# Kernel optimization log

Hardware: AMD Instinct MI355X
Metric: run time of the kernel (lower is better)

Reference implementation:

```python
import jax, jax.numpy as jnp
import numpy as np

B, T, C = 2, 2048, 1024
H = 16
DK = C // H


def setup_inputs() -> dict:
    key = jax.random.key(0)
    ks = jax.random.split(key, 5)
    x = jax.random.normal(ks[0], (B, T, C), dtype=jnp.float32)
    # causal mask, broadcastable to [B, H, T, T]; mask==0 -> -inf
    mask = jnp.tril(jnp.ones((T, T), dtype=jnp.int32))[None, None]
    s = 1.0 / np.sqrt(C)
    qkv_w = jax.random.normal(ks[1], (3 * C, C), dtype=jnp.float32) * s  # torch Linear layout [out,in]
    qkv_b = jnp.zeros((3 * C,), dtype=jnp.float32)
    out_w = jax.random.normal(ks[2], (C, C), dtype=jnp.float32) * s
    out_b = jnp.zeros((C,), dtype=jnp.float32)
    return {"x": x, "mask": mask, "qkv_w": qkv_w, "qkv_b": qkv_b,
            "out_w": out_w, "out_b": out_b}


def reference(x, mask, qkv_w, qkv_b, out_w, out_b):
    b, t, c = x.shape
    qkv = x @ qkv_w.T + qkv_b                       # [B,T,3C]
    qkv = qkv.reshape(b, t, 3, H, DK)
    q, k, v = qkv[:, :, 0], qkv[:, :, 1], qkv[:, :, 2]   # [B,T,H,DK]
    scores = jnp.einsum('bqhd,bkhd->bhqk', q, k) / np.sqrt(DK)
    scores = jnp.where(mask == 0, -jnp.inf, scores)
    attn_weights = jax.nn.softmax(scores, axis=-1)       # [B,H,T,T]
    attn_out = jnp.einsum('bhqk,bkhd->bqhd', attn_weights, v).reshape(b, t, c)
    out = attn_out @ out_w.T + out_b
    return out, attn_weights
```

## Files before the change

### kernel.cpp

```cpp
#include <hip/hip_runtime.h>
#include <hip/hip_bf16.h>

typedef short short8  __attribute__((ext_vector_type(8)));
typedef short short4v __attribute__((ext_vector_type(4)));
typedef __bf16 bf16x8 __attribute__((ext_vector_type(8)));
typedef float f32x4   __attribute__((ext_vector_type(4)));

__device__ __forceinline__ void mfma16(f32x4& d, short8 a, short8 b) {
    d = __builtin_amdgcn_mfma_f32_16x16x32_bf16(
            __builtin_bit_cast(bf16x8, a), __builtin_bit_cast(bf16x8, b), d, 0, 0, 0);
}

__device__ __forceinline__ unsigned short f2bf(float f) {
    __bf16 b = (__bf16)f;
    return __builtin_bit_cast(unsigned short, b);
}
__device__ __forceinline__ float bf2f(unsigned short us) {
    union { unsigned u; float f; } a; a.u = ((unsigned)us) << 16;
    return a.f;
}

__global__ void cvt_all(const float* __restrict__ x, const float* __restrict__ w1,
                        const float* __restrict__ w2,
                        unsigned short* __restrict__ ox, unsigned short* __restrict__ o1,
                        unsigned short* __restrict__ o2) {
    int i = blockIdx.x * 256 + threadIdx.x;
    const float* src; unsigned short* dst; int j;
    if (i < 1048576)      { src = x;  dst = ox; j = i; }
    else if (i < 1835008) { src = w1; dst = o1; j = i - 1048576; }
    else                  { src = w2; dst = o2; j = i - 1835008; }
    float4 v = ((const float4*)src)[j];
    ushort4 o;
    o.x = f2bf(v.x); o.y = f2bf(v.y); o.z = f2bf(v.z); o.w = f2bf(v.w);
    ((ushort4*)dst)[j] = o;
}

template<int OUTBF, int VTF, int BM, int BN, int MAP>
__global__ __launch_bounds__(256)
void gemm_bt(const unsigned short* __restrict__ A, const unsigned short* __restrict__ Bw,
             const float* __restrict__ bias, void* __restrict__ Cout,
             unsigned short* __restrict__ vt, unsigned short* __restrict__ khb,
             int M, int N, int K)
{
    constexpr int MM = BM / 32;
    constexpr int NN = BN / 32;
    __shared__ unsigned short As[BM * 64];
    __shared__ unsigned short Bs[BN * 64];

    const int tid  = threadIdx.x;
    const int lane = tid & 63;
    const int wid  = tid >> 6;

    int row0, col0;
    if constexpr (MAP == 1) {
        const int xcd = blockIdx.x & 7, lid = blockIdx.x >> 3;
        const int super = lid / 24, sub = lid % 24;
        row0 = ((super << 3) + (sub & 7)) << 7;
        col0 = (xcd * 3 + (sub >> 3)) << 7;
    } else {
        const int xcd = blockIdx.x & 7, lid = blockIdx.x >> 3;
        row0 = (lid >> 1) << 7;
        col0 = ((xcd << 1) + (lid & 1)) << 6;
    }
    const int wr = (wid >> 1) * (BM >> 1);
    const int wc = (wid & 1) * (BN >> 1);
    const int rl = lane & 15;
    const int g  = lane >> 4;

    f32x4 acc[MM][NN] = {};

    for (int k0 = 0; k0 < K; k0 += 64) {
        __syncthreads();
#pragma unroll
        for (int rd = 0; rd < (BM >> 5); ++rd) {
            int s  = rd * 256 + tid;
            int r  = s >> 3, cs = s & 7;
            int cg = cs ^ (r & 7);
            __builtin_amdgcn_global_load_lds(
                (__attribute__((address_space(1))) void*)(A + (size_t)(row0 + r) * K + k0 + cg * 8),
                (__attribute__((address_space(3))) void*)(As + s * 8), 16, 0, 0);
        }
#pragma unroll
        for (int rd = 0; rd < (BN >> 5); ++rd) {
            int s  = rd * 256 + tid;
            int r  = s >> 3, cs = s & 7;
            int cg = cs ^ (r & 7);
            __builtin_amdgcn_global_load_lds(
                (__attribute__((address_space(1))) void*)(Bw + (size_t)(col0 + r) * K + k0 + cg * 8),
                (__attribute__((address_space(3))) void*)(Bs + s * 8), 16, 0, 0);
        }
        __syncthreads();

#pragma unroll
        for (int h = 0; h < 2; ++h) {
            short8 af[MM], bf[NN];
#pragma unroll
            for (int m = 0; m < MM; ++m) {
                int rr = wr + m * 16 + rl;
                int ch = ((h << 2) + g) ^ (rr & 7);
                af[m] = *(const short8*)(As + rr * 64 + ch * 8);
            }
#pragma unroll
            for (int n = 0; n < NN; ++n) {
                int rr = wc + n * 16 + rl;
                int ch = ((h << 2) + g) ^ (rr & 7);
                bf[n] = *(const short8*)(Bs + rr * 64 + ch * 8);
            }
#pragma unroll
            for (int m = 0; m < MM; ++m)
#pragma unroll
                for (int n = 0; n < NN; ++n)
                    mfma16(acc[m][n], af[m], bf[n]);
        }
    }

    const int b  = row0 >> 11;
    const int tg = (row0 & 2047) + wr + (g << 2);
#pragma unroll
    for (int n = 0; n < NN; ++n) {
        int col = col0 + wc + n * 16 + rl;
        float bv = bias[col];
        if (VTF && col >= 2048) {
            int hd = col - 2048;
            unsigned short* vr = vt + ((size_t)((b << 4) + (hd >> 6)) * 64 + (hd & 63)) * 2048;
#pragma unroll
            for (int m = 0; m < MM; ++m) {
                short4v p;
#pragma unroll
                for (int r = 0; r < 4; ++r) p[r] = (short)f2bf(acc[m][n][r] + bv);
                *(short4v*)(vr + tg + m * 16) = p;
            }
        } else if (VTF && col >= 1024) {
            int hd = col - 1024;
            unsigned short* kr = khb + ((size_t)((b << 4) + (hd >> 6)) << 17) + (hd & 63);
#pragma unroll
            for (int m = 0; m < MM; ++m)
#pragma unroll
                for (int r = 0; r < 4; ++r)
                    kr[(size_t)(tg + m * 16 + r) << 6] = f2bf(acc[m][n][r] + bv);
        } else if (VTF) {
#pragma unroll
            for (int m = 0; m < MM; ++m)
#pragma unroll
                for (int r = 0; r < 4; ++r)
                    ((unsigned short*)Cout)[(size_t)(row0 + wr + m * 16 + (g << 2) + r) * 1024 + col]
                        = f2bf(acc[m][n][r] + bv);
        } else {
#pragma unroll
            for (int m = 0; m < MM; ++m) {
#pragma unroll
                for (int r = 0; r < 4; ++r) {
                    int row = row0 + wr + m * 16 + (g << 2) + r;
                    float v = acc[m][n][r] + bv;
                    if (OUTBF) ((unsigned short*)Cout)[(size_t)row * N + col] = f2bf(v);
                    else       ((float*)Cout)[(size_t)row * N + col] = v;
                }
            }
        }
    }
}

__device__ __forceinline__ int S_addr(int row, int col) {
    return (row << 11) + ((((col >> 3) ^ (row & 7))) << 3) + (col & 7);
}

__global__ __launch_bounds__(256, 2)
void attn_kernel(const unsigned short* __restrict__ qbuf,
                 const unsigned short* __restrict__ khb,
                 const unsigned short* __restrict__ vt,
                 float* __restrict__ wout,
                 unsigned short* __restrict__ aout)
{
    __shared__ unsigned short Ss[16 * 2048];
    __shared__ float part[4][16];

    const int bid = (int)(((blockIdx.x & 7) << 9) + (blockIdx.x >> 3));
    const int qt = bid & 127;
    const int bh = bid >> 7;
    const int b = bh >> 4, h = bh & 15;
    const int q0 = qt << 4;
    const int tid = threadIdx.x;
    const int wid = tid >> 6;
    const int lane = tid & 63;
    const int rl = lane & 15;
    const int g  = lane >> 4;

    int nt = (qt + 4) & ~3;
    if (nt > 128) nt = 128;
    const int ntiles = nt;
    const int KPAD = ntiles << 4;

    const unsigned short* Qb = qbuf + (size_t)((b << 11) + q0) * 1024 + (h << 6);
    short8 qf0 = *(const short8*)(Qb + rl * 1024 + g * 8);
    short8 qf1 = *(const short8*)(Qb + rl * 1024 + 32 + g * 8);

    const unsigned short* Kh = khb + ((size_t)bh << 17);

    float psum[4] = {0.f, 0.f, 0.f, 0.f};

    {
        short8 ka0, ka1, kb0, kb1;
        {
            const unsigned short* kp = Kh + (size_t)((wid * 16 + rl) << 6);
            ka0 = *(const short8*)(kp + g * 8);
            ka1 = *(const short8*)(kp + 32 + g * 8);
        }
        if (wid + 4 < ntiles) {
            const unsigned short* kp = Kh + (size_t)((((wid + 4) * 16) + rl) << 6);
            kb0 = *(const short8*)(kp + g * 8);
            kb1 = *(const short8*)(kp + 32 + g * 8);
        } else { kb0 = ka0; kb1 = ka1; }
        for (int kt = wid; kt < ntiles; kt += 4) {
            short8 kc0 = ka0, kc1 = ka1;
            ka0 = kb0; ka1 = kb1;
            if (kt + 8 < ntiles) {
                const unsigned short* kp2 = Kh + (size_t)((((kt + 8) * 16) + rl) << 6);
                kb0 = *(const short8*)(kp2 + g * 8);
                kb1 = *(const short8*)(kp2 + 32 + g * 8);
            }
            f32x4 acc = {};
            __builtin_amdgcn_s_setprio(1);
            mfma16(acc, qf0, kc0);
            mfma16(acc, qf1, kc1);
            __builtin_amdgcn_s_setprio(0);
            int col = kt * 16 + rl;
#pragma unroll
            for (int r = 0; r < 4; ++r) {
                int qrow = g * 4 + r;
                float e = (col <= q0 + qrow) ? __expf(acc[r] * 0.125f) : 0.0f;
                Ss[S_addr(qrow, col)] = f2bf(e);
                psum[r] += e;
            }
        }
    }
#pragma unroll
    for (int m = 8; m; m >>= 1)
#pragma unroll
        for (int r = 0; r < 4; ++r) psum[r] += __shfl_xor(psum[r], m);
    if (rl == 0) {
#pragma unroll
        for (int r = 0; r < 4; ++r) part[wid][g * 4 + r] = psum[r];
    }
    __syncthreads();

    f32x4 p0 = {}, p1 = {};
    const unsigned short* vrow = vt + ((size_t)(bh << 6) + wid * 16 + rl) * 2048;
    const int np = KPAD >> 6;
    const int wrow = wid + (g << 2);
    const float invw = 1.0f / (part[0][wrow] + part[1][wrow] + part[2][wrow] + part[3][wrow]);
    float* worow = wout + ((size_t)bh * 2048 + q0 + wrow) * 2048;
    short8 bv0 = *(const short8*)(vrow + (g << 3));
    short8 bv1 = *(const short8*)(vrow + 32 + (g << 3));
    for (int ic = 0; ic < 32; ++ic) {
        int colb = (ic << 6) + (rl << 2);
        f32x4 o;
        if (ic < np) {
            short8 c0 = bv0, c1 = bv1;
            if (ic + 1 < np) {
                bv0 = *(const short8*)(vrow + ((ic + 1) << 6) + (g << 3));
                bv1 = *(const short8*)(vrow + ((ic + 1) << 6) + 32 + (g << 3));
            }
            int k0c = (ic << 3) + g;
            short8 a0 = *(const short8*)(Ss + (rl << 11) + ((k0c ^ (rl & 7)) << 3));
            short8 a1 = *(const short8*)(Ss + (rl << 11) + (((k0c + 4) ^ (rl & 7)) << 3));
            __builtin_amdgcn_s_setprio(1);
            mfma16(p0, a0, c0);
            mfma16(p1, a1, c1);
            __builtin_amdgcn_s_setprio(0);
            short4v sv = *(const short4v*)(Ss + S_addr(wrow, colb));
            o[0] = bf2f((unsigned short)sv[0]) * invw;
            o[1] = bf2f((unsigned short)sv[1]) * invw;
            o[2] = bf2f((unsigned short)sv[2]) * invw;
            o[3] = bf2f((unsigned short)sv[3]) * invw;
        } else {
            o[0] = 0.f; o[1] = 0.f; o[2] = 0.f; o[3] = 0.f;
        }
        __builtin_nontemporal_store(o, (f32x4*)(worow + colb));
    }

    f32x4 pacc = p0 + p1;
#pragma unroll
    for (int r = 0; r < 4; ++r) {
        int qrow = g * 4 + r;
        float inv = 1.0f / (part[0][qrow] + part[1][qrow] + part[2][qrow] + part[3][qrow]);
        float v = pacc[r] * inv;
        aout[(size_t)((b << 11) + q0 + qrow) * 1024 + (h << 6) + wid * 16 + rl] = f2bf(v);
    }
}

extern "C" void kernel_launch(void* const* d_in, const int* in_sizes, int n_in,
                              void* d_out, int out_size, void* d_ws, size_t ws_size,
                              hipStream_t stream)
{
    const float* x     = (const float*)d_in[0];
    const float* qkv_w = (const float*)d_in[2];
    const float* qkv_b = (const float*)d_in[3];
    const float* out_w = (const float*)d_in[4];
    const float* out_b = (const float*)d_in[5];

    char* ws = (char*)d_ws;
    unsigned short* xbf   = (unsigned short*)(ws);
    unsigned short* wqkv  = (unsigned short*)(ws + 8388608);
    unsigned short* woutw = (unsigned short*)(ws + 14680064);
    unsigned short* qbuf  = (unsigned short*)(ws + 16777216);
    unsigned short* vt    = (unsigned short*)(ws + 25165824);
    unsigned short* aout  = (unsigned short*)(ws + 33554432);
    unsigned short* khb   = (unsigned short*)(ws + 41943040);

    float* out  = (float*)d_out;
    float* wout = (float*)d_out + 4194304;

    cvt_all<<<8192, 256, 0, stream>>>(x, qkv_w, out_w, xbf, wqkv, woutw);

    gemm_bt<1, 1, 128, 128, 1><<<768, 256, 0, stream>>>(xbf, wqkv, qkv_b, qbuf, vt, khb, 4096, 3072, 1024);
    attn_kernel<<<4096, 256, 0, stream>>>(qbuf, khb, vt, wout, aout);
    gemm_bt<0, 0, 128, 64, 3><<<512, 256, 0, stream>>>(aout, woutw, out_b, out, nullptr, nullptr, 4096, 1024, 1024);
}
```

Baseline: 213.4 us.

## Double-buffer GEMM K-loop with async LDS staging and reverse attention tile order

Measured after the change: 230.9 us. 8.2% more time.

```diff
diff --git a/kernel.cpp b/kernel.cpp
--- a/kernel.cpp
+++ b/kernel.cpp
@@ -18,6 +18,25 @@
 __device__ __forceinline__ float bf2f(unsigned short us) {
     union { unsigned u; float f; } a; a.u = ((unsigned)us) << 16;
     return a.f;
+}
+
+template<int ROWS>
+__device__ __forceinline__ void stage32(const unsigned short* __restrict__ src,
+                                        unsigned short* lds, int row0, int K, int k0, int tid) {
+#pragma unroll
+    for (int rd = 0; rd < (ROWS >> 6); ++rd) {
+        int s = rd * 256 + tid;
+        int p = s >> 3, cs = s & 7;
+        int cg = cs ^ (p & 7);
+        __builtin_amdgcn_global_load_lds(
+            (__attribute__((address_space(1))) void*)(src + (size_t)(row0 + 2 * p + (cg >> 2)) * K + k0 + (cg & 3) * 8),
+            (__attribute__((address_space(3))) void*)(lds + s * 8), 16, 0, 0);
+    }
+}
+__device__ __forceinline__ short8 frag32(const unsigned short* buf, int rr, int g) {
+    int p = rr >> 1;
+    int ch = (((rr & 1) << 2) | g) ^ (p & 7);
+    return *(const short8*)(buf + p * 64 + ch * 8);
 }
 
 __global__ void cvt_all(const float* __restrict__ x, const float* __restrict__ w1,
@@ -44,8 +63,9 @@
 {
     constexpr int MM = BM / 32;
     constexpr int NN = BN / 32;
-    __shared__ unsigned short As[BM * 64];
-    __shared__ unsigned short Bs[BN * 64];
+    constexpr int LPT = (BM + BN) / 64;
+    __shared__ unsigned short As[2][BM * 32];
+    __shared__ unsigned short Bs[2][BN * 32];
 
     const int tid  = threadIdx.x;
     const int lane = tid & 63;
@@ -69,48 +89,38 @@
 
     f32x4 acc[MM][NN] = {};
 
-    for (int k0 = 0; k0 < K; k0 += 64) {
-        __syncthreads();
-#pragma unroll
-        for (int rd = 0; rd < (BM >> 5); ++rd) {
-            int s  = rd * 256 + tid;
-            int r  = s >> 3, cs = s & 7;
-            int cg = cs ^ (r & 7);
-            __builtin_amdgcn_global_load_lds(
-                (__attribute__((address_space(1))) void*)(A + (size_t)(row0 + r) * K + k0 + cg * 8),
-                (__attribute__((address_space(3))) void*)(As + s * 8), 16, 0, 0);
-        }
-#pragma unroll
-        for (int rd = 0; rd < (BN >> 5); ++rd) {
-            int s  = rd * 256 + tid;
-            int r  = s >> 3, cs = s & 7;
-            int cg = cs ^ (r & 7);
-            __builtin_amdgcn_global_load_lds(
-                (__attribute__((address_space(1))) void*)(Bw + (size_t)(col0 + r) * K + k0 + cg * 8),
-                (__attribute__((address_space(3))) void*)(Bs + s * 8), 16, 0, 0);
-        }
-        __syncthreads();
-
-#pragma unroll
-        for (int h = 0; h < 2; ++h) {
-            short8 af[MM], bf[NN];
-#pragma unroll
-            for (int m = 0; m < MM; ++m) {
-                int rr = wr + m * 16 + rl;
-                int ch = ((h << 2) + g) ^ (rr & 7);
-                af[m] = *(const short8*)(As + rr * 64 + ch * 8);
-            }
-#pragma unroll
-            for (int n = 0; n < NN; ++n) {
-                int rr = wc + n * 16 + rl;
-                int ch = ((h << 2) + g) ^ (rr & 7);
-                bf[n] = *(const short8*)(Bs + rr * 64 + ch * 8);
-            }
-#pragma unroll
-            for (int m = 0; m < MM; ++m)
-#pragma unroll
-                for (int n = 0; n < NN; ++n)
-                    mfma16(acc[m][n], af[m], bf[n]);
+    const int NT = K >> 5;
+    stage32<BM>(A,  As[0], row0, K, 0,  tid);
+    stage32<BN>(Bw, Bs[0], col0, K, 0,  tid);
+    stage32<BM>(A,  As[1], row0, K, 32, tid);
+    stage32<BN>(Bw, Bs[1], col0, K, 32, tid);
+
+    for (int t = 0; t < NT; ++t) {
+        const int cur = t & 1;
+        if (t + 1 < NT) {
+            asm volatile("s_waitcnt vmcnt(%0)" :: "i"(LPT) : "memory");
+        } else {
+            asm volatile("s_waitcnt vmcnt(0)" ::: "memory");
+        }
+        __builtin_amdgcn_s_barrier();
+
+        short8 af[MM], bf[NN];
+#pragma unroll
+        for (int m = 0; m < MM; ++m) af[m] = frag32(As[cur], wr + m * 16 + rl, g);
+#pragma unroll
+        for (int n = 0; n < NN; ++n) bf[n] = frag32(Bs[cur], wc + n * 16 + rl, g);
+        __builtin_amdgcn_s_setprio(1);
+#pragma unroll
+        for (int m = 0; m < MM; ++m)
+#pragma unroll
+            for (int n = 0; n < NN; ++n)
+                mfma16(acc[m][n], af[m], bf[n]);
+        __builtin_amdgcn_s_setprio(0);
+
+        __builtin_amdgcn_s_barrier();
+        if (t + 2 < NT) {
+            stage32<BM>(A,  As[cur], row0, K, (t + 2) << 5, tid);
+            stage32<BN>(Bw, Bs[cur], col0, K, (t + 2) << 5, tid);
         }
     }
 
@@ -175,7 +185,7 @@
     __shared__ float part[4][16];
 
     const int bid = (int)(((blockIdx.x & 7) << 9) + (blockIdx.x >> 3));
-    const int qt = bid & 127;
+    const int qt = 127 - (bid & 127);
     const int bh = bid >> 7;
     const int b = bh >> 4, h = bh & 15;
     const int q0 = qt << 4;
```

## Halve attention query tile to 8 rows and shrink output-projection GEMM tiles

Applied to the files above, without the earlier changes.

New measurement: 330.0 us. +54.6%, slower.

```diff
diff --git a/kernel.cpp b/kernel.cpp
--- a/kernel.cpp
+++ b/kernel.cpp
@@ -5,6 +5,7 @@
 typedef short short4v __attribute__((ext_vector_type(4)));
 typedef __bf16 bf16x8 __attribute__((ext_vector_type(8)));
 typedef float f32x4   __attribute__((ext_vector_type(4)));
+typedef float f32x2   __attribute__((ext_vector_type(2)));
 
 __device__ __forceinline__ void mfma16(f32x4& d, short8 a, short8 b) {
     d = __builtin_amdgcn_mfma_f32_16x16x32_bf16(
@@ -59,7 +60,7 @@
         col0 = (xcd * 3 + (sub >> 3)) << 7;
     } else {
         const int xcd = blockIdx.x & 7, lid = blockIdx.x >> 3;
-        row0 = (lid >> 1) << 7;
+        row0 = (lid >> 1) << 6;
         col0 = ((xcd << 1) + (lid & 1)) << 6;
     }
     const int wr = (wid >> 1) * (BM >> 1);
@@ -164,31 +165,32 @@
     return (row << 11) + ((((col >> 3) ^ (row & 7))) << 3) + (col & 7);
 }
 
-__global__ __launch_bounds__(256, 2)
+__global__ __launch_bounds__(256, 4)
 void attn_kernel(const unsigned short* __restrict__ qbuf,
                  const unsigned short* __restrict__ khb,
                  const unsigned short* __restrict__ vt,
                  float* __restrict__ wout,
                  unsigned short* __restrict__ aout)
 {
-    __shared__ unsigned short Ss[16 * 2048];
+    __shared__ unsigned short Ss[8 * 2048];
     __shared__ float part[4][16];
 
-    const int bid = (int)(((blockIdx.x & 7) << 9) + (blockIdx.x >> 3));
-    const int qt = bid & 127;
-    const int bh = bid >> 7;
+    const int bid = (int)(((blockIdx.x & 7) << 10) + (blockIdx.x >> 3));
+    const int qt8 = bid & 255;
+    const int bh = bid >> 8;
     const int b = bh >> 4, h = bh & 15;
-    const int q0 = qt << 4;
+    const int q0 = qt8 << 3;
     const int tid = threadIdx.x;
     const int wid = tid >> 6;
     const int lane = tid & 63;
     const int rl = lane & 15;
     const int g  = lane >> 4;
 
-    int nt = (qt + 4) & ~3;
+    int nt = ((qt8 >> 1) + 4) & ~3;
     if (nt > 128) nt = 128;
     const int ntiles = nt;
     const int KPAD = ntiles << 4;
+    const int np = KPAD >> 6;
 
     const unsigned short* Qb = qbuf + (size_t)((b << 11) + q0) * 1024 + (h << 6);
     short8 qf0 = *(const short8*)(Qb + rl * 1024 + g * 8);
@@ -224,12 +226,14 @@
             mfma16(acc, qf1, kc1);
             __builtin_amdgcn_s_setprio(0);
             int col = kt * 16 + rl;
-#pragma unroll
-            for (int r = 0; r < 4; ++r) {
-                int qrow = g * 4 + r;
-                float e = (col <= q0 + qrow) ? __expf(acc[r] * 0.125f) : 0.0f;
-                Ss[S_addr(qrow, col)] = f2bf(e);
-                psum[r] += e;
+            if (g < 2) {
+#pragma unroll
+                for (int r = 0; r < 4; ++r) {
+                    int qrow = g * 4 + r;
+                    float e = (col <= q0 + qrow) ? __expf(acc[r] * 0.125f) : 0.0f;
+                    Ss[S_addr(qrow, col)] = f2bf(e);
+                    psum[r] += e;
+                }
             }
         }
     }
@@ -245,15 +249,15 @@
 
     f32x4 p0 = {}, p1 = {};
     const unsigned short* vrow = vt + ((size_t)(bh << 6) + wid * 16 + rl) * 2048;
-    const int np = KPAD >> 6;
-    const int wrow = wid + (g << 2);
-    const float invw = 1.0f / (part[0][wrow] + part[1][wrow] + part[2][wrow] + part[3][wrow]);
-    float* worow = wout + ((size_t)bh * 2048 + q0 + wrow) * 2048;
+    const int sr7 = rl & 7;
+    const int srow = tid >> 5;
+    const int scol = (tid & 31) << 1;
+    const float invw = 1.0f / (part[0][srow] + part[1][srow] + part[2][srow] + part[3][srow]);
+    float* worow = wout + ((size_t)bh * 2048 + q0 + srow) * 2048;
     short8 bv0 = *(const short8*)(vrow + (g << 3));
     short8 bv1 = *(const short8*)(vrow + 32 + (g << 3));
     for (int ic = 0; ic < 32; ++ic) {
-        int colb = (ic << 6) + (rl << 2);
-        f32x4 o;
+        f32x2 o;
         if (ic < np) {
             short8 c0 = bv0, c1 = bv1;
             if (ic + 1 < np) {
@@ -261,30 +265,30 @@
                 bv1 = *(const short8*)(vrow + ((ic + 1) << 6) + 32 + (g << 3));
             }
             int k0c = (ic << 3) + g;
-            short8 a0 = *(const short8*)(Ss + (rl << 11) + ((k0c ^ (rl & 7)) << 3));
-            short8 a1 = *(const short8*)(Ss + (rl << 11) + (((k0c + 4) ^ (rl & 7)) << 3));
+            short8 a0 = *(const short8*)(Ss + (sr7 << 11) + ((k0c ^ sr7) << 3));
+            short8 a1 = *(const short8*)(Ss + (sr7 << 11) + (((k0c + 4) ^ sr7) << 3));
             __builtin_amdgcn_s_setprio(1);
             mfma16(p0, a0, c0);
             mfma16(p1, a1, c1);
             __builtin_amdgcn_s_setprio(0);
-            short4v sv = *(const short4v*)(Ss + S_addr(wrow, colb));
-            o[0] = bf2f((unsigned short)sv[0]) * invw;
-            o[1] = bf2f((unsigned short)sv[1]) * invw;
-            o[2] = bf2f((unsigned short)sv[2]) * invw;
-            o[3] = bf2f((unsigned short)sv[3]) * invw;
+            unsigned sv = *(const unsigned*)(Ss + S_addr(srow, (ic << 6) + scol));
+            o[0] = bf2f((unsigned short)(sv & 0xffffu)) * invw;
+            o[1] = bf2f((unsigned short)(sv >> 16)) * invw;
         } else {
-            o[0] = 0.f; o[1] = 0.f; o[2] = 0.f; o[3] = 0.f;
-        }
-        __builtin_nontemporal_store(o, (f32x4*)(worow + colb));
+            o[0] = 0.f; o[1] = 0.f;
+        }
+        __builtin_nontemporal_store(o, (f32x2*)(worow + (ic << 6) + scol));
     }
 
     f32x4 pacc = p0 + p1;
-#pragma unroll
-    for (int r = 0; r < 4; ++r) {
-        int qrow = g * 4 + r;
-        float inv = 1.0f / (part[0][qrow] + part[1][qrow] + part[2][qrow] + part[3][qrow]);
-        float v = pacc[r] * inv;
-        aout[(size_t)((b << 11) + q0 + qrow) * 1024 + (h << 6) + wid * 16 + rl] = f2bf(v);
+    if (g < 2) {
+#pragma unroll
+        for (int r = 0; r < 4; ++r) {
+            int qrow = g * 4 + r;
+            float inv = 1.0f / (part[0][qrow] + part[1][qrow] + part[2][qrow] + part[3][qrow]);
+            float v = pacc[r] * inv;
+            aout[(size_t)((b << 11) + q0 + qrow) * 1024 + (h << 6) + wid * 16 + rl] = f2bf(v);
+        }
     }
 }
 
@@ -313,6 +317,6 @@
     cvt_all<<<8192, 256, 0, stream>>>(x, qkv_w, out_w, xbf, wqkv, woutw);
 
     gemm_bt<1, 1, 128, 128, 1><<<768, 256, 0, stream>>>(xbf, wqkv, qkv_b, qbuf, vt, khb, 4096, 3072, 1024);
-    attn_kernel<<<4096, 256, 0, stream>>>(qbuf, khb, vt, wout, aout);
-    gemm_bt<0, 0, 128, 64, 3><<<512, 256, 0, stream>>>(aout, woutw, out_b, out, nullptr, nullptr, 4096, 1024, 1024);
-}
+    attn_kernel<<<8192, 256, 0, stream>>>(qbuf, khb, vt, wout, aout);
+    gemm_bt<0, 0, 64, 64, 2><<<1024, 256, 0, stream>>>(aout, woutw, out_b, out, nullptr, nullptr, 4096, 1024, 1024);
+}
```
